# Kernel tuning notes

Measured on AMD Instinct MI355X. Metric: run time of the kernel, lower is better.

## Reference

```python
import jax, jax.numpy as jnp
import numpy as np

M = 0.25
GAMMA = 256.0
HARD_W = 2.0
O_P = 1.0 + M
O_N = -M
DELTA_P = 1.0 - M
DELTA_N = M
NEG_BIG = -1e30  # masked-out fill for logsumexp (finite to keep grads NaN-free)


def setup_inputs() -> dict:
    key = jax.random.key(0)
    k1, k2 = jax.random.split(key)
    inputs = jax.random.normal(k1, (4096, 512), dtype=jnp.float32)
    targets = jax.random.randint(k2, (4096,), 0, 64, dtype=jnp.int64)
    return {"inputs": inputs, "targets": targets}


def reference(inputs, targets):
    n = inputs.shape[0]
    x = inputs / jnp.linalg.norm(inputs, axis=1, keepdims=True)  # L2 normalize
    sim = x @ x.T                                                # [n, n]

    same = targets[:, None] == targets[None, :]
    eye = jnp.eye(n, dtype=bool)
    pos_mask = same & ~eye
    neg_mask = ~same
    npos = pos_mask.sum(axis=1)
    nneg = neg_mask.sum(axis=1)

    sim_d = jax.lax.stop_gradient(sim)  # alphas are detached in the original
    alpha_p = jax.nn.relu(O_P - sim_d)
    alpha_n = jax.nn.relu(sim_d - O_N)

    # hard mining: scale alpha at hardest positive (min sim) / hardest negative (max sim)
    idx = jnp.arange(n)
    hard_p = jnp.argmin(jnp.where(pos_mask, sim_d, jnp.inf), axis=1)
    hard_n = jnp.argmax(jnp.where(neg_mask, sim_d, -jnp.inf), axis=1)
    hit_p = (idx[None, :] == hard_p[:, None]) & (npos > 1)[:, None]
    hit_n = (idx[None, :] == hard_n[:, None]) & (nneg > 1)[:, None]
    alpha_p = alpha_p * jnp.where(hit_p, HARD_W, 1.0)
    alpha_n = alpha_n * jnp.where(hit_n, HARD_W, 1.0)

    pos_term = jnp.where(pos_mask, -GAMMA * alpha_p * (sim - DELTA_P), NEG_BIG)
    neg_term = jnp.where(neg_mask, GAMMA * alpha_n * (sim - DELTA_N), NEG_BIG)
    lse_p = jax.nn.logsumexp(pos_term, axis=1)
    lse_n = jax.nn.logsumexp(neg_term, axis=1)

    valid = (npos > 0) & (nneg > 0)
    per_row = jnp.where(valid, jax.nn.softplus(lse_p + lse_n), 0.0)
    n_valid = jnp.maximum(valid.sum(), 1)
    return per_row.sum() / n_valid.astype(per_row.dtype)
```

## Files before the change

kernel.cpp:

```cpp
#include <hip/hip_runtime.h>


#define GAMMA_ 256.0f
#define MASKT_  (-1.0e4f)
#define MINITP_ (-1.0e4f)
#define MASKP_  (-3.0e4f)

constexpr int N_ = 4096;
constexpr int D_ = 512;
constexpr int AST_ = 520;
constexpr int CCH_ = 16;

typedef __bf16 bf16x8 __attribute__((ext_vector_type(8)));
typedef float  f32x4  __attribute__((ext_vector_type(4)));
typedef const unsigned int __attribute__((address_space(1)))* gp_t;
typedef unsigned int       __attribute__((address_space(3)))* lp_t;

__device__ __forceinline__ float pos_q(float s) {
    float d = s - 1.0f;
    return fmaf(d * d, 256.0f, -16.0f);
}
__device__ __forceinline__ float neg_q(float s) {
    float q = fmaf(s * s, 256.0f, -16.0f);
    return (s >= -0.25f) ? q : 0.0f;
}
__device__ __forceinline__ void lse_merge(float m2, float S2, float& m, float& S) {
    float mm = fmaxf(m, m2);
    S = S * __expf(m - mm) + S2 * __expf(m2 - mm);
    m = mm;
}
__device__ __forceinline__ unsigned short f2bf(float f) {
    unsigned int u = __float_as_uint(f);
    unsigned int r = u + 0x7FFFu + ((u >> 16) & 1u);
    return (unsigned short)(r >> 16);
}

__global__ __launch_bounds__(256) void k_norm(const float* __restrict__ in,
                                              unsigned short* __restrict__ xb,
                                              float* __restrict__ acc) {
    const int row  = blockIdx.x * 4 + (threadIdx.x >> 6);
    const int lane = threadIdx.x & 63;
    const float4* src = (const float4*)(in + (size_t)row * D_) + lane * 2;
    float4 a = src[0], b = src[1];
    float ss = a.x*a.x + a.y*a.y + a.z*a.z + a.w*a.w
             + b.x*b.x + b.y*b.y + b.z*b.z + b.w*b.w;
    #pragma unroll
    for (int d = 32; d >= 1; d >>= 1) ss += __shfl_xor(ss, d);
    float rn = 1.0f / sqrtf(ss);
    float v[8] = {a.x, a.y, a.z, a.w, b.x, b.y, b.z, b.w};
    union { uint4 u; unsigned short us[8]; } pk;
    #pragma unroll
    for (int k = 0; k < 8; ++k) pk.us[k] = f2bf(v[k] * rn);
    *((uint4*)(xb + (size_t)row * D_) + lane) = pk.u;
    if (blockIdx.x == 0 && threadIdx.x < 4) acc[threadIdx.x] = 0.0f;
}

__global__ __launch_bounds__(256, 2) void k_mainH(const unsigned short* __restrict__ xb,
                                                  const int* __restrict__ tg,
                                                  float* __restrict__ part) {
    constexpr int NST = 16;
    __shared__ __align__(16) unsigned short Bs[2][16][AST_];

    const int tid  = threadIdx.x;
    const int wave = tid >> 6, lane = tid & 63;
    const int n16  = lane & 15, quad = lane >> 4;
    const int rg   = (int)blockIdx.x >> 4;
    const int cc   = (int)blockIdx.x & 15;
    const int rowBase = rg * 128 + wave * 32;
    const int colBase = cc * 256;

    bf16x8 af0[16], af1[16];
    {
        const bf16x8* ap0 = (const bf16x8*)(xb + (size_t)(rowBase + n16) * D_ + quad * 8);
        const bf16x8* ap1 = (const bf16x8*)(xb + (size_t)(rowBase + 16 + n16) * D_ + quad * 8);
        #pragma unroll
        for (int kk = 0; kk < 16; ++kk) { af0[kk] = ap0[kk * 4]; af1[kk] = ap1[kk * 4]; }
    }
    int tr[8];
    #pragma unroll
    for (int g = 0; g < 2; ++g)
        #pragma unroll
        for (int r = 0; r < 4; ++r) tr[g * 4 + r] = tg[rowBase + g * 16 + quad * 4 + r];

    float m_p[8], S_p[8], m_n[8], S_n[8], mxn[8];
    #pragma unroll
    for (int i = 0; i < 8; ++i) {
        m_p[i] = MINITP_; S_p[i] = 0.f; m_n[i] = 0.f; S_n[i] = 0.f; mxn[i] = -2.0f;
    }

    const char* gstage = (const char*)xb + (size_t)colBase * 1024 + lane * 16;

    #pragma unroll
    for (int p = 0; p < 4; ++p) {
        int j = p * 4 + wave;
        __builtin_amdgcn_global_load_lds((gp_t)(const void*)(gstage + j * 1024),
                                         (lp_t)(void*)&Bs[0][j][0], 16, 0, 0);
    }
    int tc_cur = tg[colBase + n16];

    auto epi = [&](const f32x4& a0, const f32x4& a1, int tcv, bool withDiag, int base) {
        #pragma unroll
        for (int r = 0; r < 4; ++r) {
            float sim = a0[r] + a1[r];
            bool samec = (tr[base + r] == tcv);
            float u = samec ? (sim - 1.0f) : sim;
            float t = fmaf(u * u, 256.0f, -16.0f);
            if (!samec && sim < -0.25f) t = 0.0f;
            if (withDiag && n16 == quad * 4 + r) t = MASKP_;
            float ms = samec ? m_p[base + r] : m_n[base + r];
            if (t > ms) {
                float scl = __expf(ms - t);
                if (samec) { S_p[base + r] = fmaf(S_p[base + r], scl, 1.0f); m_p[base + r] = t; }
                else       { S_n[base + r] = fmaf(S_n[base + r], scl, 1.0f); m_n[base + r] = t; }
            } else {
                float e = __expf(t - ms);
                S_p[base + r] += samec ? e : 0.0f;
                S_n[base + r] += samec ? 0.0f : e;
            }
            mxn[base + r] = fmaxf(mxn[base + r], samec ? -2.0f : sim);
        }
    };

    #pragma unroll 1
    for (int s = 0; s < NST; ++s) {
        const int b = s & 1;
        const int j0 = colBase + s * 16;
        __syncthreads();

        if (s + 1 < NST) {
            const char* g2 = gstage + (size_t)(s + 1) * 16 * 1024;
            #pragma unroll
            for (int p = 0; p < 4; ++p) {
                int j = p * 4 + wave;
                __builtin_amdgcn_global_load_lds((gp_t)(const void*)(g2 + j * 1024),
                                                 (lp_t)(void*)&Bs[b ^ 1][j][0], 16, 0, 0);
            }
        }
        int tc_nxt = (s + 1 < NST) ? tg[colBase + (s + 1) * 16 + n16] : 0;

        f32x4 a0 = {0.f, 0.f, 0.f, 0.f}, a1 = {0.f, 0.f, 0.f, 0.f};
        f32x4 a2 = {0.f, 0.f, 0.f, 0.f}, a3 = {0.f, 0.f, 0.f, 0.f};
        #pragma unroll
        for (int kk = 0; kk < 8; ++kk) {
            bf16x8 bf0 = *(const bf16x8*)&Bs[b][n16][(2 * kk) * 32 + quad * 8];
            bf16x8 bf1 = *(const bf16x8*)&Bs[b][n16][(2 * kk + 1) * 32 + quad * 8];
            a0 = __builtin_amdgcn_mfma_f32_16x16x32_bf16(af0[2 * kk],     bf0, a0, 0, 0, 0);
            a1 = __builtin_amdgcn_mfma_f32_16x16x32_bf16(af0[2 * kk + 1], bf1, a1, 0, 0, 0);
            a2 = __builtin_amdgcn_mfma_f32_16x16x32_bf16(af1[2 * kk],     bf0, a2, 0, 0, 0);
            a3 = __builtin_amdgcn_mfma_f32_16x16x32_bf16(af1[2 * kk + 1], bf1, a3, 0, 0, 0);
        }

        if (j0 == rowBase)      epi(a0, a1, tc_cur, true,  0);
        else                    epi(a0, a1, tc_cur, false, 0);
        if (j0 == rowBase + 16) epi(a2, a3, tc_cur, true,  4);
        else                    epi(a2, a3, tc_cur, false, 4);
        tc_cur = tc_nxt;
    }

    #pragma unroll
    for (int i = 0; i < 8; ++i) {
        #pragma unroll
        for (int d = 1; d <= 8; d <<= 1) {
            lse_merge(__shfl_xor(m_p[i], d), __shfl_xor(S_p[i], d), m_p[i], S_p[i]);
            lse_merge(__shfl_xor(m_n[i], d), __shfl_xor(S_n[i], d), m_n[i], S_n[i]);
            mxn[i] = fmaxf(mxn[i], __shfl_xor(mxn[i], d));
        }
    }
    if (n16 == 0) {
        #pragma unroll
        for (int g = 0; g < 2; ++g)
            #pragma unroll
            for (int r = 0; r < 4; ++r) {
                int i = g * 4 + r;
                ((float4*)part)[(size_t)(rowBase + g * 16 + quad * 4 + r) * CCH_ + cc] =
                    make_float4(m_p[i], S_p[i], mxn[i], S_n[i]);
            }
    }
}

__global__ __launch_bounds__(256) void k_reduceF(const float* __restrict__ part,
                                                 const int* __restrict__ tg,
                                                 float* __restrict__ acc,
                                                 float* __restrict__ out) {
    __shared__ int hist[64];
    const int tid = threadIdx.x;
    if (tid < 64) hist[tid] = 0;
    __syncthreads();
    for (int i = tid; i < N_; i += 256) atomicAdd(&hist[tg[i]], 1);
    __syncthreads();

    const int row = blockIdx.x * 256 + tid;
    const float4* P = (const float4*)part + (size_t)row * CCH_;
    float M_p = MINITP_, Sp = 0.f, M_n = 0.f, Sn = 0.f, mxn = -2.0f;
    #pragma unroll
    for (int c = 0; c < CCH_; ++c) {
        float4 a = P[c];
        lse_merge(a.x, a.y, M_p, Sp);
        float mn = (a.z > -1.5f) ? fmaxf(neg_q(a.z), 0.0f) : 0.0f;
        lse_merge(mn, a.w, M_n, Sn);
        mxn = fmaxf(mxn, a.z);
    }
    const int cnt = hist[tg[row]];
    float np2 = (float)(cnt - 1), nn2 = (float)(N_ - cnt);
    float loss = 0.f, vld = 0.f;
    if (np2 > 0.5f && nn2 > 0.5f) {
        if (np2 > 1.5f) {
            float t1 = M_p, t2 = 2.0f * t1;
            float mm = fmaxf(M_p, t2);
            Sp = Sp * __expf(M_p - mm) + __expf(t2 - mm) - __expf(t1 - mm);
            M_p = mm;
        }
        if (nn2 > 1.5f) {
            float t1 = neg_q(mxn), t2 = 2.0f * t1;
            float mm = fmaxf(M_n, t2);
            Sn = Sn * __expf(M_n - mm) + __expf(t2 - mm) - __expf(t1 - mm);
            M_n = mm;
        }
        float z = (M_p + __logf(Sp)) + (M_n + __logf(Sn));
        loss = fmaxf(z, 0.0f) + log1pf(__expf(-fabsf(z)));
        vld = 1.0f;
    }
    #pragma unroll
    for (int d = 32; d >= 1; d >>= 1) { loss += __shfl_xor(loss, d); vld += __shfl_xor(vld, d); }
    if ((tid & 63) == 0) { atomicAdd(&acc[0], loss); atomicAdd(&acc[1], vld); }

    __syncthreads();
    if (tid == 0) {
        __threadfence();
        int old = atomicAdd((int*)(acc + 2), 1);
        if (old == (int)gridDim.x - 1) {
            float ls = atomicAdd(&acc[0], 0.0f);
            float lv = atomicAdd(&acc[1], 0.0f);
            out[0] = ls / fmaxf(lv, 1.0f);
        }
    }
}

__global__ void k_final(const float* __restrict__ acc, float* __restrict__ out) {
    if (threadIdx.x == 0) out[0] = acc[0] / fmaxf(acc[1], 1.0f);
}

__global__ void k_sentinel(float* __restrict__ out) {
    if (threadIdx.x == 0) out[0] = -12345.0f;
}

__global__ __launch_bounds__(1024, 4) void k_main3(const unsigned short* __restrict__ xb,
                                                   const int* __restrict__ tg,
                                                   float* __restrict__ acc_g) {
    __shared__ __align__(16) unsigned short As[16 * AST_];
    __shared__ float sm[16][16][8];
    const int tid  = threadIdx.x;
    const int wave = tid >> 6, lane = tid & 63;
    const int n16  = lane & 15, quad = lane >> 4;
    const int rowBase = blockIdx.x * 16;
    {
        int row = tid >> 6, c = tid & 63;
        *(uint4*)&As[row * AST_ + c * 8] =
            *(const uint4*)(xb + (size_t)(rowBase + row) * D_ + c * 8);
    }
    int ir[4], tr[4];
    #pragma unroll
    for (int r = 0; r < 4; ++r) { ir[r] = rowBase + quad * 4 + r; tr[r] = tg[ir[r]]; }
    float m_p[4], S_p[4], m_n[4], S_n[4], mnp[4], mxn[4], sc[4];
    #pragma unroll
    for (int r = 0; r < 4; ++r) {
        m_p[r] = 0.f; S_p[r] = 0.f; m_n[r] = 0.f; S_n[r] = 0.f;
        mnp[r] = 2.0f; mxn[r] = -2.0f; sc[r] = 0.f;
    }
    __syncthreads();
    const unsigned short* Af = &As[n16 * AST_ + quad * 8];
    #pragma unroll 1
    for (int t = wave; t < N_ / 16; t += 16) {
        const int jcol = t * 16 + n16;
        const int tc = tg[jcol];
        const bf16x8* bp = (const bf16x8*)(xb + (size_t)jcol * D_ + quad * 8);
        bf16x8 bf[16];
        #pragma unroll
        for (int kk = 0; kk < 16; ++kk) bf[kk] = bp[kk * 4];
        f32x4 a0 = {0.f, 0.f, 0.f, 0.f}, a1 = {0.f, 0.f, 0.f, 0.f};
        #pragma unroll
        for (int kk = 0; kk < 8; ++kk) {
            bf16x8 af0 = *(const bf16x8*)(Af + (2 * kk) * 32);
            bf16x8 af1 = *(const bf16x8*)(Af + (2 * kk + 1) * 32);
            a0 = __builtin_amdgcn_mfma_f32_16x16x32_bf16(af0, bf[2 * kk],     a0, 0, 0, 0);
            a1 = __builtin_amdgcn_mfma_f32_16x16x32_bf16(af1, bf[2 * kk + 1], a1, 0, 0, 0);
        }
        #pragma unroll
        for (int r = 0; r < 4; ++r) {
            float s = a0[r] + a1[r];
            bool samec = (tr[r] == tc);
            bool posm  = samec && (jcol != ir[r]);
            float tp = posm  ? pos_q(s) : MASKT_;
            float tn = samec ? MASKT_ : neg_q(s);
            float mm = fmaxf(m_p[r], tp);
            S_p[r] = S_p[r] * __expf(m_p[r] - mm) + __expf(tp - mm); m_p[r] = mm;
            mm = fmaxf(m_n[r], tn);
            S_n[r] = S_n[r] * __expf(m_n[r] - mm) + __expf(tn - mm); m_n[r] = mm;
            sc[r] += samec ? 1.0f : 0.0f;
            mnp[r] = fminf(mnp[r], posm ? s : 2.0f);
            mxn[r] = fmaxf(mxn[r], samec ? -2.0f : s);
        }
    }
    #pragma unroll
    for (int r = 0; r < 4; ++r) {
        #pragma unroll
        for (int d = 1; d <= 8; d <<= 1) {
            lse_merge(__shfl_xor(m_p[r], d), __shfl_xor(S_p[r], d), m_p[r], S_p[r]);
            lse_merge(__shfl_xor(m_n[r], d), __shfl_xor(S_n[r], d), m_n[r], S_n[r]);
            mnp[r] = fminf(mnp[r], __shfl_xor(mnp[r], d));
            mxn[r] = fmaxf(mxn[r], __shfl_xor(mxn[r], d));
            sc[r] += __shfl_xor(sc[r], d);
        }
    }
    if (n16 == 0) {
        #pragma unroll
        for (int r = 0; r < 4; ++r) {
            float* q = sm[wave][quad * 4 + r];
            q[0] = m_p[r]; q[1] = S_p[r]; q[2] = m_n[r]; q[3] = S_n[r];
            q[4] = mnp[r]; q[5] = mxn[r]; q[6] = sc[r];
        }
    }
    __syncthreads();
    if (tid < 64) {
        const int L = tid & 15;
        float m_p2 = 0.f, S_p2 = 0.f, m_n2 = 0.f, S_n2 = 0.f;
        float mnp2 = 2.0f, mxn2 = -2.0f, sct = 0.f;
        #pragma unroll
        for (int w = 0; w < 16; ++w) {
            const float* q = sm[w][L];
            lse_merge(q[0], q[1], m_p2, S_p2);
            lse_merge(q[2], q[3], m_n2, S_n2);
            mnp2 = fminf(mnp2, q[4]); mxn2 = fmaxf(mxn2, q[5]);
            sct += q[6];
        }
        float loss = 0.f, vld = 0.f;
        float np2 = sct - 1.0f, nn2 = (float)N_ - sct;
        if (tid < 16 && np2 > 0.5f && nn2 > 0.5f) {
            if (np2 > 1.5f) {
                float t1 = pos_q(mnp2), t2 = 2.0f * t1;
                float mm = fmaxf(m_p2, t2);
                S_p2 = S_p2 * __expf(m_p2 - mm) + __expf(t2 - mm) - __expf(t1 - mm);
                m_p2 = mm;
            }
            if (nn2 > 1.5f) {
                float t1 = neg_q(mxn2), t2 = 2.0f * t1;
                float mm = fmaxf(m_n2, t2);
                S_n2 = S_n2 * __expf(m_n2 - mm) + __expf(t2 - mm) - __expf(t1 - mm);
                m_n2 = mm;
            }
            float z = (m_p2 + __logf(S_p2)) + (m_n2 + __logf(S_n2));
            loss = fmaxf(z, 0.0f) + log1pf(__expf(-fabsf(z)));
            vld = 1.0f;
        }
        #pragma unroll
        for (int d = 32; d >= 1; d >>= 1) {
            loss += __shfl_xor(loss, d); vld += __shfl_xor(vld, d);
        }
        if (tid == 0) { atomicAdd(&acc_g[0], loss); atomicAdd(&acc_g[1], vld); }
    }
}

extern "C" void kernel_launch(void* const* d_in, const int* in_sizes, int n_in,
                              void* d_out, int out_size, void* d_ws, size_t ws_size,
                              hipStream_t stream) {
    const float* in = (const float*)d_in[0];
    const int*   tg = (const int*)d_in[1];
    constexpr size_t MB = 1024 * 1024;
    unsigned short* xb = (unsigned short*)d_ws;

    if (ws_size >= 5 * MB + 64) {
        float* part = (float*)((char*)d_ws + 4 * MB);
        float* acc  = (float*)((char*)d_ws + 5 * MB);
        hipLaunchKernelGGL(k_norm,    dim3(N_ / 4),    dim3(256), 0, stream, in, xb, acc);
        hipLaunchKernelGGL(k_mainH,   dim3(32 * CCH_), dim3(256), 0, stream, xb, tg, part);
        hipLaunchKernelGGL(k_reduceF, dim3(N_ / 256),  dim3(256), 0, stream, part, tg, acc,
                           (float*)d_out);
    } else if (ws_size >= 4 * MB + 64) {
        float* acc = (float*)((char*)d_ws + 4 * MB);
        hipLaunchKernelGGL(k_norm,  dim3(N_ / 4),  dim3(256),  0, stream, in, xb, acc);
        hipLaunchKernelGGL(k_main3, dim3(N_ / 16), dim3(1024), 0, stream, xb, tg, acc);
        hipLaunchKernelGGL(k_final, dim3(1),       dim3(64),   0, stream, acc, (float*)d_out);
    } else {
        hipLaunchKernelGGL(k_sentinel, dim3(1), dim3(64), 0, stream, (float*)d_out);
    }
}
```

Measured before the change: 110.2 us.

## Load B tiles directly from global into registers, dropping LDS staging and barriers

Each wave now loads its column-block B fragments straight from global memory into registers, split into low and high halves that are prefetched for the next step while MFMAs consume the other half. The shared-memory double buffer, the global_load_lds staging and the per-step __syncthreads are removed. This cuts LDS traffic and block-wide synchronisation, but every wave in the block now fetches the same B data itself (four times more L2/global traffic), and register pressure rises from the 16 extra bf16x8 registers.

```diff
diff --git a/kernel.cpp b/kernel.cpp
--- a/kernel.cpp
+++ b/kernel.cpp
@@ -13,8 +13,6 @@
 
 typedef __bf16 bf16x8 __attribute__((ext_vector_type(8)));
 typedef float  f32x4  __attribute__((ext_vector_type(4)));
-typedef const unsigned int __attribute__((address_space(1)))* gp_t;
-typedef unsigned int       __attribute__((address_space(3)))* lp_t;
 
 __device__ __forceinline__ float pos_q(float s) {
     float d = s - 1.0f;
@@ -55,12 +53,10 @@
     if (blockIdx.x == 0 && threadIdx.x < 4) acc[threadIdx.x] = 0.0f;
 }
 
-__global__ __launch_bounds__(256, 2) void k_mainH(const unsigned short* __restrict__ xb,
+__global__ __launch_bounds__(256, 2) void k_mainI(const unsigned short* __restrict__ xb,
                                                   const int* __restrict__ tg,
                                                   float* __restrict__ part) {
     constexpr int NST = 16;
-    __shared__ __align__(16) unsigned short Bs[2][16][AST_];
-
     const int tid  = threadIdx.x;
     const int wave = tid >> 6, lane = tid & 63;
     const int n16  = lane & 15, quad = lane >> 4;
@@ -88,14 +84,13 @@
         m_p[i] = MINITP_; S_p[i] = 0.f; m_n[i] = 0.f; S_n[i] = 0.f; mxn[i] = -2.0f;
     }
 
-    const char* gstage = (const char*)xb + (size_t)colBase * 1024 + lane * 16;
-
-    #pragma unroll
-    for (int p = 0; p < 4; ++p) {
-        int j = p * 4 + wave;
-        __builtin_amdgcn_global_load_lds((gp_t)(const void*)(gstage + j * 1024),
-                                         (lp_t)(void*)&Bs[0][j][0], 16, 0, 0);
-    }
+    const bf16x8* bp = (const bf16x8*)(xb + (size_t)(colBase + n16) * D_ + quad * 8);
+
+    bf16x8 bl[8], bh[8];
+    #pragma unroll
+    for (int f = 0; f < 8; ++f) bl[f] = bp[f * 4];
+    #pragma unroll
+    for (int f = 0; f < 8; ++f) bh[f] = bp[(8 + f) * 4];
     int tc_cur = tg[colBase + n16];
 
     auto epi = [&](const f32x4& a0, const f32x4& a1, int tcv, bool withDiag, int base) {
@@ -123,31 +118,35 @@
 
     #pragma unroll 1
     for (int s = 0; s < NST; ++s) {
-        const int b = s & 1;
         const int j0 = colBase + s * 16;
-        __syncthreads();
-
-        if (s + 1 < NST) {
-            const char* g2 = gstage + (size_t)(s + 1) * 16 * 1024;
-            #pragma unroll
-            for (int p = 0; p < 4; ++p) {
-                int j = p * 4 + wave;
-                __builtin_amdgcn_global_load_lds((gp_t)(const void*)(g2 + j * 1024),
-                                                 (lp_t)(void*)&Bs[b ^ 1][j][0], 16, 0, 0);
-            }
-        }
         int tc_nxt = (s + 1 < NST) ? tg[colBase + (s + 1) * 16 + n16] : 0;
 
         f32x4 a0 = {0.f, 0.f, 0.f, 0.f}, a1 = {0.f, 0.f, 0.f, 0.f};
         f32x4 a2 = {0.f, 0.f, 0.f, 0.f}, a3 = {0.f, 0.f, 0.f, 0.f};
-        #pragma unroll
-        for (int kk = 0; kk < 8; ++kk) {
-            bf16x8 bf0 = *(const bf16x8*)&Bs[b][n16][(2 * kk) * 32 + quad * 8];
-            bf16x8 bf1 = *(const bf16x8*)&Bs[b][n16][(2 * kk + 1) * 32 + quad * 8];
-            a0 = __builtin_amdgcn_mfma_f32_16x16x32_bf16(af0[2 * kk],     bf0, a0, 0, 0, 0);
-            a1 = __builtin_amdgcn_mfma_f32_16x16x32_bf16(af0[2 * kk + 1], bf1, a1, 0, 0, 0);
-            a2 = __builtin_amdgcn_mfma_f32_16x16x32_bf16(af1[2 * kk],     bf0, a2, 0, 0, 0);
-            a3 = __builtin_amdgcn_mfma_f32_16x16x32_bf16(af1[2 * kk + 1], bf1, a3, 0, 0, 0);
+
+        #pragma unroll
+        for (int f = 0; f < 8; f += 2) {
+            a0 = __builtin_amdgcn_mfma_f32_16x16x32_bf16(af0[f],     bl[f],     a0, 0, 0, 0);
+            a2 = __builtin_amdgcn_mfma_f32_16x16x32_bf16(af1[f],     bl[f],     a2, 0, 0, 0);
+            a1 = __builtin_amdgcn_mfma_f32_16x16x32_bf16(af0[f + 1], bl[f + 1], a1, 0, 0, 0);
+            a3 = __builtin_amdgcn_mfma_f32_16x16x32_bf16(af1[f + 1], bl[f + 1], a3, 0, 0, 0);
+        }
+        if (s + 1 < NST) {
+            const bf16x8* bpn = bp + (size_t)(s + 1) * 1024;
+            #pragma unroll
+            for (int f = 0; f < 8; ++f) bl[f] = bpn[f * 4];
+        }
+        #pragma unroll
+        for (int f = 8; f < 16; f += 2) {
+            a0 = __builtin_amdgcn_mfma_f32_16x16x32_bf16(af0[f],     bh[f - 8], a0, 0, 0, 0);
+            a2 = __builtin_amdgcn_mfma_f32_16x16x32_bf16(af1[f],     bh[f - 8], a2, 0, 0, 0);
+            a1 = __builtin_amdgcn_mfma_f32_16x16x32_bf16(af0[f + 1], bh[f - 7], a1, 0, 0, 0);
+            a3 = __builtin_amdgcn_mfma_f32_16x16x32_bf16(af1[f + 1], bh[f - 7], a3, 0, 0, 0);
+        }
+        if (s + 1 < NST) {
+            const bf16x8* bpn = bp + (size_t)(s + 1) * 1024;
+            #pragma unroll
+            for (int f = 0; f < 8; ++f) bh[f] = bpn[(8 + f) * 4];
         }
 
         if (j0 == rowBase)      epi(a0, a1, tc_cur, true,  0);
@@ -372,7 +371,7 @@
         float* part = (float*)((char*)d_ws + 4 * MB);
         float* acc  = (float*)((char*)d_ws + 5 * MB);
         hipLaunchKernelGGL(k_norm,    dim3(N_ / 4),    dim3(256), 0, stream, in, xb, acc);
-        hipLaunchKernelGGL(k_mainH,   dim3(32 * CCH_), dim3(256), 0, stream, xb, tg, part);
+        hipLaunchKernelGGL(k_mainI,   dim3(32 * CCH_), dim3(256), 0, stream, xb, tg, part);
         hipLaunchKernelGGL(k_reduceF, dim3(N_ / 256),  dim3(256), 0, stream, part, tg, acc,
                            (float*)d_out);
     } else if (ws_size >= 4 * MB + 64) {
```

Measured after the change: 159.6 us. +44.8%, slower.
